# Kernel tuning notes

Hardware: AMD Instinct MI355X
Metric: run time of the kernel (lower is better)

Reference implementation:

```python
import jax, jax.numpy as jnp
import numpy as np
import math

B, S, D = 2, 512, 768
N_HEADS, HEAD = 12, 64
ALPHA = 32.0


def setup_inputs() -> dict:
    key = jax.random.key(0)
    ks = jax.random.split(key, 12)
    w_scale = 1.0 / math.sqrt(D)
    return {
        "hidden_states": jax.random.normal(ks[0], (B, S, D), jnp.float32),
        "attention_mask": jnp.zeros((B, 1, 1, S), jnp.float32),
        "rel_pos": jax.random.normal(ks[1], (B, S, S, HEAD), jnp.float32),
        "rel_2d_pos": jax.random.normal(ks[2], (B, S, S, HEAD), jnp.float32),
        "rel_2d_angle": jax.random.normal(ks[3], (B, S, S, HEAD), jnp.float32),
        "Wq": jax.random.normal(ks[4], (D, D), jnp.float32) * w_scale,
        "bq": jnp.zeros((D,), jnp.float32),
        "Wk": jax.random.normal(ks[5], (D, D), jnp.float32) * w_scale,
        "bk": jnp.zeros((D,), jnp.float32),
        "Wv": jax.random.normal(ks[6], (D, D), jnp.float32) * w_scale,
        "bv": jnp.zeros((D,), jnp.float32),
    }


def _heads(x):
    # (B,S,D) -> (B,N,S,HEAD)
    b, s, _ = x.shape
    return x.reshape(b, s, N_HEADS, HEAD).transpose(0, 2, 1, 3)


def reference(hidden_states, attention_mask, rel_pos, rel_2d_pos, rel_2d_angle,
              Wq, bq, Wk, bk, Wv, bv):
    q = _heads(hidden_states @ Wq.T + bq)
    k = _heads(hidden_states @ Wk.T + bk)
    v = _heads(hidden_states @ Wv.T + bv)

    qs = q / math.sqrt(HEAD)  # scaled query, (B,N,S,HEAD)
    scores = jnp.einsum('bnsh,bnkh->bnsk', qs, k)
    scores = scores + jnp.einsum('bnsh,bskh->bnsk', qs, rel_pos)
    scores = scores + jnp.einsum('bnsh,bskh->bnsk', qs, rel_2d_pos)
    scores = scores + jnp.einsum('bnsh,bskh->bnsk', qs, rel_2d_angle)
    scores = scores + attention_mask

    # cogview (PB-Relax) softmax: subtract per-row max of scores/alpha, rescale
    scaled = scores / ALPHA
    m = jnp.max(scaled, axis=-1, keepdims=True)
    probs = jax.nn.softmax((scaled - m) * ALPHA, axis=-1)

    ctx = jnp.einsum('bnsk,bnkh->bsnh', probs, v)  # (B,S,N,HEAD)
    return ctx.reshape(ctx.shape[0], ctx.shape[1], N_HEADS * HEAD)
```

## Files before the change

### kernel.cpp

```cpp
#include <hip/hip_runtime.h>

typedef __attribute__((ext_vector_type(8))) short short8;
typedef __attribute__((ext_vector_type(4))) float f32x4;

#define B_ 2
#define S_ 512
#define D_ 768
#define NH 12
#define HD 64

__device__ inline short f2bf(float f) {
    union { float f; unsigned u; } v; v.f = f;
    unsigned r = v.u + 0x7fffu + ((v.u >> 16) & 1u);
    return (short)(r >> 16);
}

__global__ __launch_bounds__(256) void qkv_gemm(
    const float* __restrict__ hidden,
    const float* __restrict__ Wq, const float* __restrict__ Wk, const float* __restrict__ Wv,
    const float* __restrict__ bq, const float* __restrict__ bk, const float* __restrict__ bv,
    short* __restrict__ qbf, short* __restrict__ kbf, float* __restrict__ vws)
{
    __shared__ short hs[64 * 72];
    __shared__ short wt[64 * 72];

    const int mt = blockIdx.x, nt = blockIdx.y, mat = blockIdx.z;
    const int m0 = mt * 64, n0 = nt * 64;
    const float* W    = (mat == 0) ? Wq : ((mat == 1) ? Wk : Wv);
    const float* bias = (mat == 0) ? bq : ((mat == 1) ? bk : bv);

    const int tid = threadIdx.x;
    const int w = tid >> 6, l = tid & 63;
    const int sr = tid >> 2, sc = (tid & 3) * 16;

    f32x4 acc[4];
    #pragma unroll
    for (int i = 0; i < 4; ++i) acc[i] = (f32x4){0.f, 0.f, 0.f, 0.f};

    const int arow = (w * 16 + (l & 15)) * 72 + (l >> 4) * 8;

    for (int kt = 0; kt < 12; ++kt) {
        const int d0 = kt * 64;
        if (kt) __syncthreads();
        {
            const float4* sa = (const float4*)(hidden + (size_t)(m0 + sr) * D_ + d0 + sc);
            float4 x0 = sa[0], x1 = sa[1], x2 = sa[2], x3 = sa[3];
            short8 p0 = {f2bf(x0.x), f2bf(x0.y), f2bf(x0.z), f2bf(x0.w),
                         f2bf(x1.x), f2bf(x1.y), f2bf(x1.z), f2bf(x1.w)};
            short8 p1 = {f2bf(x2.x), f2bf(x2.y), f2bf(x2.z), f2bf(x2.w),
                         f2bf(x3.x), f2bf(x3.y), f2bf(x3.z), f2bf(x3.w)};
            *(short8*)&hs[sr * 72 + sc]     = p0;
            *(short8*)&hs[sr * 72 + sc + 8] = p1;
            const float4* sb = (const float4*)(W + (size_t)(n0 + sr) * D_ + d0 + sc);
            float4 y0 = sb[0], y1 = sb[1], y2 = sb[2], y3 = sb[3];
            short8 q0 = {f2bf(y0.x), f2bf(y0.y), f2bf(y0.z), f2bf(y0.w),
                         f2bf(y1.x), f2bf(y1.y), f2bf(y1.z), f2bf(y1.w)};
            short8 q1 = {f2bf(y2.x), f2bf(y2.y), f2bf(y2.z), f2bf(y2.w),
                         f2bf(y3.x), f2bf(y3.y), f2bf(y3.z), f2bf(y3.w)};
            *(short8*)&wt[sr * 72 + sc]     = q0;
            *(short8*)&wt[sr * 72 + sc + 8] = q1;
        }
        __syncthreads();
        short8 a0 = *(const short8*)&hs[arow];
        short8 a1 = *(const short8*)&hs[arow + 32];
        #pragma unroll
        for (int ct = 0; ct < 4; ++ct) {
            const int brow = (ct * 16 + (l & 15)) * 72 + (l >> 4) * 8;
            short8 b0 = *(const short8*)&wt[brow];
            short8 b1 = *(const short8*)&wt[brow + 32];
            acc[ct] = __builtin_amdgcn_mfma_f32_16x16x32_bf16(a0, b0, acc[ct], 0, 0, 0);
            acc[ct] = __builtin_amdgcn_mfma_f32_16x16x32_bf16(a1, b1, acc[ct], 0, 0, 0);
        }
    }

    #pragma unroll
    for (int ct = 0; ct < 4; ++ct) {
        #pragma unroll
        for (int rr = 0; rr < 4; ++rr) {
            const int m_l = w * 16 + (l >> 4) * 4 + rr;
            const int n_l = ct * 16 + (l & 15);
            const int m = m0 + m_l;
            const int b = m >> 9, s = m & 511;
            float v = acc[ct][rr] + bias[n0 + n_l];
            const size_t dst = (((size_t)(b * NH + nt) * S_) + s) * HD + n_l;
            if (mat == 0)      qbf[dst] = f2bf(v * 0.125f);
            else if (mat == 1) kbf[dst] = f2bf(v);
            else               vws[dst] = v;
        }
    }
}

__global__ __launch_bounds__(256) void score_qk(
    const short* __restrict__ qbf, const short* __restrict__ kbf,
    const float* __restrict__ mask, float* __restrict__ scores)
{
    __shared__ short qa[64 * 72];
    __shared__ short kb[64 * 72];

    const int st = blockIdx.x, ktile = blockIdx.y, z = blockIdx.z;
    const int b = z / NH, n = z % NH;
    const int s0 = st * 64, k0 = ktile * 64;
    const int tid = threadIdx.x;
    const int w = tid >> 6, l = tid & 63;
    const int sr = tid >> 2, sc = (tid & 3) * 16;

    {
        const short8* sa = (const short8*)(qbf + (((size_t)(b * NH + n) * S_) + s0 + sr) * HD + sc);
        *(short8*)&qa[sr * 72 + sc]     = sa[0];
        *(short8*)&qa[sr * 72 + sc + 8] = sa[1];
        const short8* sb = (const short8*)(kbf + (((size_t)(b * NH + n) * S_) + k0 + sr) * HD + sc);
        *(short8*)&kb[sr * 72 + sc]     = sb[0];
        *(short8*)&kb[sr * 72 + sc + 8] = sb[1];
    }
    __syncthreads();

    f32x4 acc[4];
    #pragma unroll
    for (int i = 0; i < 4; ++i) acc[i] = (f32x4){0.f, 0.f, 0.f, 0.f};

    const int arow = (w * 16 + (l & 15)) * 72 + (l >> 4) * 8;
    short8 a0 = *(const short8*)&qa[arow];
    short8 a1 = *(const short8*)&qa[arow + 32];
    #pragma unroll
    for (int ct = 0; ct < 4; ++ct) {
        const int brow = (ct * 16 + (l & 15)) * 72 + (l >> 4) * 8;
        short8 b0 = *(const short8*)&kb[brow];
        short8 b1 = *(const short8*)&kb[brow + 32];
        acc[ct] = __builtin_amdgcn_mfma_f32_16x16x32_bf16(a0, b0, acc[ct], 0, 0, 0);
        acc[ct] = __builtin_amdgcn_mfma_f32_16x16x32_bf16(a1, b1, acc[ct], 0, 0, 0);
    }

    #pragma unroll
    for (int ct = 0; ct < 4; ++ct) {
        const float mv = mask[b * S_ + k0 + ct * 16 + (l & 15)];
        #pragma unroll
        for (int rr = 0; rr < 4; ++rr) {
            const int s_l = w * 16 + (l >> 4) * 4 + rr;
            scores[(((size_t)(b * NH + n) * S_) + s0 + s_l) * S_ + k0 + ct * 16 + (l & 15)]
                = acc[ct][rr] + mv;
        }
    }
}

__global__ __launch_bounds__(256, 4) void score_rel(
    const short* __restrict__ qbf,
    const float* __restrict__ rel1, const float* __restrict__ rel2, const float* __restrict__ rel3,
    float* __restrict__ scores)
{
    const int kt = blockIdx.x;
    const int s  = blockIdx.y;
    const int b  = blockIdx.z;
    const int tid = threadIdx.x;
    const int w = tid >> 6, l = tid & 63;

    const int rowsel = l & 15;
    const int hc     = (l >> 4) * 8;

    const int kc = kt * 4 + w;
    const size_t rbase = ((size_t)(b * S_ + s)) * S_ * HD;
    const size_t ro = rbase + (size_t)(kc * 16 + rowsel) * HD + hc;

    float4 p0a = *(const float4*)(rel1 + ro);
    float4 p0b = *(const float4*)(rel1 + ro + 4);
    float4 q0a = *(const float4*)(rel1 + ro + 32);
    float4 q0b = *(const float4*)(rel1 + ro + 36);
    float4 p1a = *(const float4*)(rel2 + ro);
    float4 p1b = *(const float4*)(rel2 + ro + 4);
    float4 q1a = *(const float4*)(rel2 + ro + 32);
    float4 q1b = *(const float4*)(rel2 + ro + 36);
    float4 p2a = *(const float4*)(rel3 + ro);
    float4 p2b = *(const float4*)(rel3 + ro + 4);
    float4 q2a = *(const float4*)(rel3 + ro + 32);
    float4 q2b = *(const float4*)(rel3 + ro + 36);

    short8 a0 = {0, 0, 0, 0, 0, 0, 0, 0};
    short8 a1 = {0, 0, 0, 0, 0, 0, 0, 0};
    if (rowsel < NH) {
        const short* qp = qbf + (((size_t)(b * NH + rowsel) * S_) + s) * HD;
        a0 = *(const short8*)(qp + hc);
        a1 = *(const short8*)(qp + hc + 32);
    }

    short8 b0 = {
        f2bf(p0a.x + p1a.x + p2a.x), f2bf(p0a.y + p1a.y + p2a.y),
        f2bf(p0a.z + p1a.z + p2a.z), f2bf(p0a.w + p1a.w + p2a.w),
        f2bf(p0b.x + p1b.x + p2b.x), f2bf(p0b.y + p1b.y + p2b.y),
        f2bf(p0b.z + p1b.z + p2b.z), f2bf(p0b.w + p1b.w + p2b.w)};
    short8 b1 = {
        f2bf(q0a.x + q1a.x + q2a.x), f2bf(q0a.y + q1a.y + q2a.y),
        f2bf(q0a.z + q1a.z + q2a.z), f2bf(q0a.w + q1a.w + q2a.w),
        f2bf(q0b.x + q1b.x + q2b.x), f2bf(q0b.y + q1b.y + q2b.y),
        f2bf(q0b.z + q1b.z + q2b.z), f2bf(q0b.w + q1b.w + q2b.w)};

    f32x4 acc = (f32x4){0.f, 0.f, 0.f, 0.f};
    acc = __builtin_amdgcn_mfma_f32_16x16x32_bf16(a0, b0, acc, 0, 0, 0);
    acc = __builtin_amdgcn_mfma_f32_16x16x32_bf16(a1, b1, acc, 0, 0, 0);

    const int kg = kc * 16 + rowsel;
    #pragma unroll
    for (int rr = 0; rr < 4; ++rr) {
        const int n = (l >> 4) * 4 + rr;
        if (n < NH) {
            float* p = scores + (((size_t)(b * NH + n) * S_) + s) * S_ + kg;
            *p += acc[rr];
        }
    }
}

__global__ __launch_bounds__(256) void smpv_kernel(
    const float* __restrict__ scores, const float* __restrict__ vws,
    float* __restrict__ out)
{
    __shared__ float sc[16][512];

    const int st  = blockIdx.x;
    const int n   = blockIdx.y;
    const int b   = blockIdx.z;
    const int s0  = st * 16;
    const int tid = threadIdx.x;

    const size_t base = (((size_t)(b * NH + n) * S_) + s0) * S_;

    #pragma unroll
    for (int j = 0; j < 8; ++j) {
        const int fidx = j * 256 + tid;
        const int row  = fidx >> 7;
        const int c4   = fidx & 127;
        float4 v = *(const float4*)(scores + base + (size_t)row * S_ + c4 * 4);
        *(float4*)&sc[row][c4 * 4] = v;
    }
    __syncthreads();

    const int w = tid >> 6, lane = tid & 63;

    for (int r = 0; r < 4; ++r) {
        const int row = w * 4 + r;
        float vals[8];
        float m = -1e30f;
        #pragma unroll
        for (int i = 0; i < 8; ++i) { vals[i] = sc[row][lane + 64 * i]; m = fmaxf(m, vals[i]); }
        #pragma unroll
        for (int off = 32; off >= 1; off >>= 1) m = fmaxf(m, __shfl_xor(m, off));
        float sum = 0.f;
        #pragma unroll
        for (int i = 0; i < 8; ++i) { vals[i] = __expf(vals[i] - m); sum += vals[i]; }
        #pragma unroll
        for (int off = 32; off >= 1; off >>= 1) sum += __shfl_xor(sum, off);
        const float inv = 1.0f / sum;
        #pragma unroll
        for (int i = 0; i < 8; ++i) sc[row][lane + 64 * i] = vals[i] * inv;
    }
    __syncthreads();

    float acc[4] = {0.f, 0.f, 0.f, 0.f};
    const float* vb = vws + (((size_t)(b * NH + n) * S_)) * HD + lane;
    for (int k = 0; k < S_; k += 4) {
        const float v0 = vb[(size_t)(k + 0) * HD];
        const float v1 = vb[(size_t)(k + 1) * HD];
        const float v2 = vb[(size_t)(k + 2) * HD];
        const float v3 = vb[(size_t)(k + 3) * HD];
        #pragma unroll
        for (int r = 0; r < 4; ++r) {
            float4 p = *(const float4*)&sc[w * 4 + r][k];
            acc[r] += p.x * v0 + p.y * v1 + p.z * v2 + p.w * v3;
        }
    }
    #pragma unroll
    for (int r = 0; r < 4; ++r)
        out[((size_t)(b * S_ + s0 + w * 4 + r)) * D_ + n * HD + lane] = acc[r];
}

extern "C" void kernel_launch(void* const* d_in, const int* in_sizes, int n_in,
                              void* d_out, int out_size, void* d_ws, size_t ws_size,
                              hipStream_t stream) {
    const float* hidden = (const float*)d_in[0];
    const float* mask   = (const float*)d_in[1];
    const float* rel1   = (const float*)d_in[2];
    const float* rel2   = (const float*)d_in[3];
    const float* rel3   = (const float*)d_in[4];
    const float* Wq     = (const float*)d_in[5];
    const float* bq     = (const float*)d_in[6];
    const float* Wk     = (const float*)d_in[7];
    const float* bk     = (const float*)d_in[8];
    const float* Wv     = (const float*)d_in[9];
    const float* bv     = (const float*)d_in[10];
    float* out = (float*)d_out;

    const size_t per = (size_t)B_ * NH * S_ * HD;
    short* qbf    = (short*)d_ws;
    short* kbf    = qbf + per;
    float* vws    = (float*)(kbf + per);
    float* scores = vws + per;

    qkv_gemm<<<dim3(16, 12, 3), 256, 0, stream>>>(hidden, Wq, Wk, Wv, bq, bk, bv, qbf, kbf, vws);
    score_qk<<<dim3(8, 8, 24), 256, 0, stream>>>(qbf, kbf, mask, scores);
    score_rel<<<dim3(8, S_, B_), 256, 0, stream>>>(qbf, rel1, rel2, rel3, scores);
    smpv_kernel<<<dim3(S_ / 16, NH, B_), 256, 0, stream>>>(scores, vws, out);
}
```

Before: 156.6 us.

## Fuse QK score computation into softmax-PV kernel and store rel scores separately

Removes the separate score_qk kernel. The QK^T MFMA tiles are now computed inside the softmax/PV kernel, which writes them to shared memory and then adds the relative-position scores and the mask before the softmax. score_rel now writes its results to a separate buffer laid out as (b,s,n,k) with plain stores instead of doing read-modify-write on the global scores array. This saves one launch and the global scores write/read round-trip. In exchange, each softmax block recomputes QK from global K without shared-memory staging, and the shared-memory row is padded to 520.

```diff
diff --git a/kernel.cpp b/kernel.cpp
--- a/kernel.cpp
+++ b/kernel.cpp
@@ -90,62 +90,10 @@
     }
 }
 
-__global__ __launch_bounds__(256) void score_qk(
-    const short* __restrict__ qbf, const short* __restrict__ kbf,
-    const float* __restrict__ mask, float* __restrict__ scores)
-{
-    __shared__ short qa[64 * 72];
-    __shared__ short kb[64 * 72];
-
-    const int st = blockIdx.x, ktile = blockIdx.y, z = blockIdx.z;
-    const int b = z / NH, n = z % NH;
-    const int s0 = st * 64, k0 = ktile * 64;
-    const int tid = threadIdx.x;
-    const int w = tid >> 6, l = tid & 63;
-    const int sr = tid >> 2, sc = (tid & 3) * 16;
-
-    {
-        const short8* sa = (const short8*)(qbf + (((size_t)(b * NH + n) * S_) + s0 + sr) * HD + sc);
-        *(short8*)&qa[sr * 72 + sc]     = sa[0];
-        *(short8*)&qa[sr * 72 + sc + 8] = sa[1];
-        const short8* sb = (const short8*)(kbf + (((size_t)(b * NH + n) * S_) + k0 + sr) * HD + sc);
-        *(short8*)&kb[sr * 72 + sc]     = sb[0];
-        *(short8*)&kb[sr * 72 + sc + 8] = sb[1];
-    }
-    __syncthreads();
-
-    f32x4 acc[4];
-    #pragma unroll
-    for (int i = 0; i < 4; ++i) acc[i] = (f32x4){0.f, 0.f, 0.f, 0.f};
-
-    const int arow = (w * 16 + (l & 15)) * 72 + (l >> 4) * 8;
-    short8 a0 = *(const short8*)&qa[arow];
-    short8 a1 = *(const short8*)&qa[arow + 32];
-    #pragma unroll
-    for (int ct = 0; ct < 4; ++ct) {
-        const int brow = (ct * 16 + (l & 15)) * 72 + (l >> 4) * 8;
-        short8 b0 = *(const short8*)&kb[brow];
-        short8 b1 = *(const short8*)&kb[brow + 32];
-        acc[ct] = __builtin_amdgcn_mfma_f32_16x16x32_bf16(a0, b0, acc[ct], 0, 0, 0);
-        acc[ct] = __builtin_amdgcn_mfma_f32_16x16x32_bf16(a1, b1, acc[ct], 0, 0, 0);
-    }
-
-    #pragma unroll
-    for (int ct = 0; ct < 4; ++ct) {
-        const float mv = mask[b * S_ + k0 + ct * 16 + (l & 15)];
-        #pragma unroll
-        for (int rr = 0; rr < 4; ++rr) {
-            const int s_l = w * 16 + (l >> 4) * 4 + rr;
-            scores[(((size_t)(b * NH + n) * S_) + s0 + s_l) * S_ + k0 + ct * 16 + (l & 15)]
-                = acc[ct][rr] + mv;
-        }
-    }
-}
-
-__global__ __launch_bounds__(256, 4) void score_rel(
+__global__ __launch_bounds__(256) void score_rel(
     const short* __restrict__ qbf,
     const float* __restrict__ rel1, const float* __restrict__ rel2, const float* __restrict__ rel3,
-    float* __restrict__ scores)
+    float* __restrict__ relsc)
 {
     const int kt = blockIdx.x;
     const int s  = blockIdx.y;
@@ -200,39 +148,71 @@
     #pragma unroll
     for (int rr = 0; rr < 4; ++rr) {
         const int n = (l >> 4) * 4 + rr;
-        if (n < NH) {
-            float* p = scores + (((size_t)(b * NH + n) * S_) + s) * S_ + kg;
-            *p += acc[rr];
-        }
-    }
-}
-
-__global__ __launch_bounds__(256) void smpv_kernel(
-    const float* __restrict__ scores, const float* __restrict__ vws,
-    float* __restrict__ out)
+        if (n < NH)
+            relsc[(((size_t)(b * S_ + s)) * NH + n) * S_ + kg] = acc[rr];
+    }
+}
+
+__global__ __launch_bounds__(256) void smqkpv(
+    const short* __restrict__ qbf, const short* __restrict__ kbf,
+    const float* __restrict__ relsc, const float* __restrict__ mask,
+    const float* __restrict__ vws, float* __restrict__ out)
 {
-    __shared__ float sc[16][512];
+    __shared__ float sc[16][520];
 
     const int st  = blockIdx.x;
     const int n   = blockIdx.y;
     const int b   = blockIdx.z;
     const int s0  = st * 16;
     const int tid = threadIdx.x;
-
-    const size_t base = (((size_t)(b * NH + n) * S_) + s0) * S_;
+    const int w = tid >> 6, l = tid & 63;
+
+    const int arow = l & 15;
+    const int g    = l >> 4;
+
+    const short* qp = qbf + (((size_t)(b * NH + n) * S_) + s0 + arow) * HD + g * 8;
+    short8 a0 = *(const short8*)(qp);
+    short8 a1 = *(const short8*)(qp + 32);
+
+    f32x4 acc[8];
+    #pragma unroll
+    for (int t = 0; t < 8; ++t) acc[t] = (f32x4){0.f, 0.f, 0.f, 0.f};
+
+    #pragma unroll
+    for (int t = 0; t < 8; ++t) {
+        const int k0 = (w * 8 + t) * 16;
+        const short* kp = kbf + (((size_t)(b * NH + n) * S_) + k0 + arow) * HD + g * 8;
+        short8 b0 = *(const short8*)(kp);
+        short8 b1 = *(const short8*)(kp + 32);
+        acc[t] = __builtin_amdgcn_mfma_f32_16x16x32_bf16(a0, b0, acc[t], 0, 0, 0);
+        acc[t] = __builtin_amdgcn_mfma_f32_16x16x32_bf16(a1, b1, acc[t], 0, 0, 0);
+    }
+
+    #pragma unroll
+    for (int t = 0; t < 8; ++t) {
+        const int k0 = (w * 8 + t) * 16;
+        #pragma unroll
+        for (int rr = 0; rr < 4; ++rr)
+            sc[g * 4 + rr][k0 + arow] = acc[t][rr];
+    }
+    __syncthreads();
 
     #pragma unroll
     for (int j = 0; j < 8; ++j) {
         const int fidx = j * 256 + tid;
         const int row  = fidx >> 7;
-        const int c4   = fidx & 127;
-        float4 v = *(const float4*)(scores + base + (size_t)row * S_ + c4 * 4);
-        *(float4*)&sc[row][c4 * 4] = v;
+        const int c4   = (fidx & 127) * 4;
+        float4 r = *(const float4*)(relsc +
+                    (((size_t)(b * S_ + s0 + row)) * NH + n) * S_ + c4);
+        float4 mk = *(const float4*)(mask + b * S_ + c4);
+        float4 cur = *(const float4*)&sc[row][c4];
+        cur.x += r.x + mk.x; cur.y += r.y + mk.y;
+        cur.z += r.z + mk.z; cur.w += r.w + mk.w;
+        *(float4*)&sc[row][c4] = cur;
     }
     __syncthreads();
 
-    const int w = tid >> 6, lane = tid & 63;
-
+    const int lane = l;
     for (int r = 0; r < 4; ++r) {
         const int row = w * 4 + r;
         float vals[8];
@@ -252,7 +232,7 @@
     }
     __syncthreads();
 
-    float acc[4] = {0.f, 0.f, 0.f, 0.f};
+    float pacc[4] = {0.f, 0.f, 0.f, 0.f};
     const float* vb = vws + (((size_t)(b * NH + n) * S_)) * HD + lane;
     for (int k = 0; k < S_; k += 4) {
         const float v0 = vb[(size_t)(k + 0) * HD];
@@ -262,12 +242,12 @@
         #pragma unroll
         for (int r = 0; r < 4; ++r) {
             float4 p = *(const float4*)&sc[w * 4 + r][k];
-            acc[r] += p.x * v0 + p.y * v1 + p.z * v2 + p.w * v3;
+            pacc[r] += p.x * v0 + p.y * v1 + p.z * v2 + p.w * v3;
         }
     }
     #pragma unroll
     for (int r = 0; r < 4; ++r)
-        out[((size_t)(b * S_ + s0 + w * 4 + r)) * D_ + n * HD + lane] = acc[r];
+        out[((size_t)(b * S_ + s0 + w * 4 + r)) * D_ + n * HD + lane] = pacc[r];
 }
 
 extern "C" void kernel_launch(void* const* d_in, const int* in_sizes, int n_in,
@@ -287,13 +267,12 @@
     float* out = (float*)d_out;
 
     const size_t per = (size_t)B_ * NH * S_ * HD;
-    short* qbf    = (short*)d_ws;
-    short* kbf    = qbf + per;
-    float* vws    = (float*)(kbf + per);
-    float* scores = vws + per;
+    short* qbf   = (short*)d_ws;
+    short* kbf   = qbf + per;
+    float* vws   = (float*)(kbf + per);
+    float* relsc = vws + per;
 
     qkv_gemm<<<dim3(16, 12, 3), 256, 0, stream>>>(hidden, Wq, Wk, Wv, bq, bk, bv, qbf, kbf, vws);
-    score_qk<<<dim3(8, 8, 24), 256, 0, stream>>>(qbf, kbf, mask, scores);
-    score_rel<<<dim3(8, S_, B_), 256, 0, stream>>>(qbf, rel1, rel2, rel3, scores);
-    smpv_kernel<<<dim3(S_ / 16, NH, B_), 256, 0, stream>>>(scores, vws, out);
-}
+    score_rel<<<dim3(8, S_, B_), 256, 0, stream>>>(qbf, rel1, rel2, rel3, relsc);
+    smqkpv<<<dim3(S_ / 16, NH, B_), 256, 0, stream>>>(qbf, kbf, relsc, mask, vws, out);
+}
```

Measured after the change: 147.5 us. 5.8% less time.
